# Kernel tuning notes

Measured on AMD Instinct MI355X. Metric: run time of the kernel, lower is better.

## Reference

```python
import jax, jax.numpy as jnp
import numpy as np

EPS = 1e-12
SIMILARITY = 'dot'  # non-tensor forward arg, closed over


def setup_inputs() -> dict:
    key = jax.random.key(0)
    k1, k2, k3, k4 = jax.random.split(key, 4)
    N, M, D = 4096, 8192, 512
    x = jax.random.normal(k1, (N, D), dtype=jnp.float32)
    x_n = jax.random.normal(k2, (M, D), dtype=jnp.float32)
    # Linear(D, 3) params
    W = jax.random.normal(k3, (3, D), dtype=jnp.float32) * (1.0 / np.sqrt(D))
    bias = jax.random.normal(k4, (3,), dtype=jnp.float32) * 0.01
    return {"x": x, "x_n": x_n, "W": W, "bias": bias}


def _sim_matrix(x, x_n, similarity):
    if similarity == 'l2':
        d2 = (jnp.sum(x * x, 1)[:, None] - 2.0 * (x @ x_n.T)
              + jnp.sum(x_n * x_n, 1)[None, :])
        return -jnp.sqrt(jnp.maximum(d2, 0.0))
    elif similarity == 'l1':
        return -jnp.sum(jnp.abs(x[:, None, :] - x_n[None, :, :]), axis=-1)
    elif similarity == 'dot':
        return (x @ x_n.T) / x.shape[1]
    elif similarity == 'cos':
        xn = x / jnp.linalg.norm(x, axis=1, keepdims=True)
        yn = x_n / jnp.linalg.norm(x_n, axis=1, keepdims=True)
        return xn @ yn.T


def reference(x, x_n, W, bias):
    # pointwise params from a Linear(D,3)+Sigmoid head, clamped to (eps, 1-eps)
    p = jnp.clip(jax.nn.sigmoid(x @ W.T + bias), EPS, 1.0 - EPS)  # [N,3]
    a = p[:, 0:1]
    b = p[:, 1:2]
    s = p[:, 2:3]
    b = a + b * (1.0 - a)

    sim = _sim_matrix(x, x_n, SIMILARITY)                # [N,M]
    smin = jnp.min(sim, axis=1, keepdims=True)
    smax = jnp.max(sim, axis=1, keepdims=True)
    sim_norm = (sim - smin) / (smax - smin)

    # x != x_n -> plain row max (torch.equal branch is False)
    top_sims = jnp.max(sim_norm, axis=1, keepdims=True)  # [N,1]
    a = jnp.minimum(a, top_sims) - EPS

    num = jnp.maximum(jnp.abs(sim_norm - a) ** (1.0 / s), EPS)
    denom = num + jnp.maximum(jnp.abs(b - sim_norm) ** (1.0 / s), EPS)
    soft_mask = num / denom

    lo = sim_norm < a
    hi = sim_norm > b
    soft_mask = jnp.where(lo, 0.0, jnp.where(hi, 1.0, soft_mask))
    # safe log: masked-to-0 entries give -inf forward, zero grad (matches torch)
    safe = jnp.where(lo, 1.0, soft_mask)
    log_mask = jnp.where(lo, -jnp.inf, jnp.log(safe))
    return sim + log_mask
```

## Files before the change

kernel.cpp:

```cpp
#include <hip/hip_runtime.h>
#include <hip/hip_fp16.h>
#include <math.h>

#define EPSF 1e-12f
#define NEG_HUGE (-1e30f)

typedef _Float16 half8_t __attribute__((ext_vector_type(8)));
typedef _Float16 half4_t __attribute__((ext_vector_type(4)));
typedef float floatx4 __attribute__((ext_vector_type(4)));

__device__ __forceinline__ float sigmoid_stable(float v) {
    if (v >= 0.0f) {
        return 1.0f / (1.0f + expf(-v));
    } else {
        float e = expf(v);
        return e / (1.0f + e);
    }
}

__global__ __launch_bounds__(64) void row_params_kernel(
    const float* __restrict__ x, const float* __restrict__ W,
    const float* __restrict__ bias,
    float* __restrict__ aeff, float* __restrict__ bnew, float* __restrict__ tinv)
{
    const int r = blockIdx.x;
    const int l = threadIdx.x;
    const float* xr = x + (size_t)r * 512;
    float s0 = 0.0f, s1 = 0.0f, s2 = 0.0f;
#pragma unroll
    for (int i = 0; i < 8; ++i) {
        int e = l * 8 + i;
        float xv = xr[e];
        s0 = fmaf(xv, W[e], s0);
        s1 = fmaf(xv, W[512 + e], s1);
        s2 = fmaf(xv, W[1024 + e], s2);
    }
#pragma unroll
    for (int off = 32; off > 0; off >>= 1) {
        s0 += __shfl_xor(s0, off);
        s1 += __shfl_xor(s1, off);
        s2 += __shfl_xor(s2, off);
    }
    if (l == 0) {
        float p0 = fminf(fmaxf(sigmoid_stable(s0 + bias[0]), EPSF), 1.0f);
        float p1 = fminf(fmaxf(sigmoid_stable(s1 + bias[1]), EPSF), 1.0f);
        float p2 = fminf(fmaxf(sigmoid_stable(s2 + bias[2]), EPSF), 1.0f);
        float b = p0 + p1 * (1.0f - p0);
        float ae = fminf(p0, 1.0f) - EPSF;
        aeff[r] = ae;
        bnew[r] = b;
        tinv[r] = 1.0f / p2;
    }
}

__global__ __launch_bounds__(256) void split_both_kernel(
    const float* __restrict__ x, const float* __restrict__ xn,
    _Float16* __restrict__ A2, _Float16* __restrict__ B2)
{
    int idx = blockIdx.x * 256 + threadIdx.x;
    int row = idx >> 7;
    int c = (idx & 127) << 2;
    const float* src;
    _Float16* dst;
    bool isB;
    if (row < 4096) {
        src = x + (size_t)row * 512 + c;
        dst = A2 + (size_t)row * 1536 + c;
        isB = false;
    } else {
        int r = row - 4096;
        src = xn + (size_t)r * 512 + c;
        dst = B2 + (size_t)r * 1536 + c;
        isB = true;
    }
    float4 v = *(const float4*)src;
    _Float16 h0 = (_Float16)v.x, h1 = (_Float16)v.y,
             h2 = (_Float16)v.z, h3 = (_Float16)v.w;
    half4_t hv = {h0, h1, h2, h3};
    half4_t lv = {(_Float16)(v.x - (float)h0), (_Float16)(v.y - (float)h1),
                  (_Float16)(v.z - (float)h2), (_Float16)(v.w - (float)h3)};
    *(half4_t*)(dst) = hv;
    *(half4_t*)(dst + 512)  = isB ? lv : hv;
    *(half4_t*)(dst + 1024) = isB ? hv : lv;
}

#define VMW_(N) asm volatile("s_waitcnt vmcnt(" #N ")" ::: "memory")
#define VMW(N) VMW_(N)
#define BARR() __builtin_amdgcn_s_barrier()

__device__ __forceinline__ void gload16(const _Float16* g, _Float16* l) {
    __builtin_amdgcn_global_load_lds(
        (const __attribute__((address_space(1))) unsigned int*)g,
        (__attribute__((address_space(3))) unsigned int*)l, 16, 0, 0);
}

#define RD_A4(dst, QQ, qd)                                                      \
    dst[0] = *(const half8_t*)(lds + (QQ)*16384 + ArdW + (2*(qd))*1024 + g0);   \
    dst[1] = *(const half8_t*)(lds + (QQ)*16384 + ArdW + (2*(qd))*1024 + g1);   \
    dst[2] = *(const half8_t*)(lds + (QQ)*16384 + ArdW + (2*(qd)+1)*1024 + g0); \
    dst[3] = *(const half8_t*)(lds + (QQ)*16384 + ArdW + (2*(qd)+1)*1024 + g1);

#define RD_B8(dst, QQ)                                                          \
    _Pragma("unroll")                                                           \
    for (int fn = 0; fn < 4; ++fn) {                                            \
        dst[2*fn]   = *(const half8_t*)(lds + (QQ)*16384 + BrdW + fn*1024 + g0);\
        dst[2*fn+1] = *(const half8_t*)(lds + (QQ)*16384 + BrdW + fn*1024 + g1);\
    }

#define MFMA_Q(qd, af, bf)                                                      \
    __builtin_amdgcn_s_setprio(1);                                              \
    _Pragma("unroll")                                                           \
    for (int fn = 0; fn < 4; ++fn) {                                            \
        acc[2*(qd)][fn] = __builtin_amdgcn_mfma_f32_16x16x32_f16(               \
            af[0], bf[2*fn], acc[2*(qd)][fn], 0, 0, 0);                         \
        acc[2*(qd)][fn] = __builtin_amdgcn_mfma_f32_16x16x32_f16(               \
            af[1], bf[2*fn+1], acc[2*(qd)][fn], 0, 0, 0);                       \
        acc[2*(qd)+1][fn] = __builtin_amdgcn_mfma_f32_16x16x32_f16(             \
            af[2], bf[2*fn], acc[2*(qd)+1][fn], 0, 0, 0);                       \
        acc[2*(qd)+1][fn] = __builtin_amdgcn_mfma_f32_16x16x32_f16(             \
            af[3], bf[2*fn+1], acc[2*(qd)+1][fn], 0, 0, 0);                     \
    }                                                                           \
    __builtin_amdgcn_s_setprio(0);

__global__ __launch_bounds__(512, 2) void mfma_gemm256_kernel(
    const _Float16* __restrict__ A, const _Float16* __restrict__ B,
    float* __restrict__ C,
    float* __restrict__ pmin, float* __restrict__ pmax)
{
    constexpr int KP = 1536;
    constexpr int NN = 8192;
    __shared__ __align__(16) _Float16 lds[65536];

    const int tid = threadIdx.x;
    const int wave = tid >> 6, lane = tid & 63;
    const int bx = blockIdx.x;
    const int by = blockIdx.y;
    const int wm = (wave >> 2) * 128;
    const int wn = (wave & 3) * 64;

    const int rl = lane & 15, lq = lane >> 4;
    const int rx7 = lane & 7;
    const int lrow = lane >> 3, gph = lane & 7;
    const int glog = gph ^ lrow;

    const _Float16* Bg = B + (size_t)(bx * 256 + wave * 8 + lrow) * KP + glog * 8;
    const _Float16* Ag = A + (size_t)(by * 256 + ((wave & 4) ? 128 : 0)
                                      + (wave & 3) * 8 + lrow) * KP + glog * 8;
    const int BdstW = 32768 + (wave * 8) * 64;
    const int AdstW = (((wave & 4) ? 128 : 0) + (wave & 3) * 8) * 64;
    const int ArdW = (wm + rl) * 64;
    const int BrdW = 32768 + (wn + rl) * 64;
    const int g0 = (lq ^ rx7) * 8;
    const int g1 = ((4 + lq) ^ rx7) * 8;

    floatx4 acc[8][4] = {};
    half8_t a0[4], a1[4], bA[8], bB[8];

    auto stageB = [&](int u, int qn, int kn) {
        gload16(Bg + (size_t)u * (64 * KP) + kn * 64,
                lds + qn * 16384 + BdstW + u * 4096);
    };
    auto stageA = [&](int s, int qn, int kn) {
        gload16(Ag + (size_t)s * (32 * KP) + kn * 64,
                lds + qn * 16384 + AdstW + s * 2048);
    };

#pragma unroll
    for (int u = 0; u < 4; ++u) stageB(u, 0, 0);
#pragma unroll
    for (int s = 0; s < 4; ++s) stageA(s, 0, 0);
    VMW(3);
    BARR();
    RD_B8(bA, 0); RD_A4(a0, 0, 0);
    stageB(0, 1, 1); stageB(1, 1, 1);
    VMW(4);
    BARR();

    for (int kt = 0; kt < 22; kt += 2) {
        const int k1 = kt + 1, k2 = kt + 2, k3 = kt + 3;
        RD_A4(a1, 0, 1); stageB(2, 1, k1); stageB(3, 1, k1);
        MFMA_Q(0, a0, bA); VMW(5); BARR();
        RD_A4(a0, 0, 2); stageA(0, 1, k1); stageA(1, 1, k1);
        MFMA_Q(1, a1, bA); VMW(6); BARR();
        RD_A4(a1, 0, 3); stageA(2, 1, k1); stageA(3, 1, k1);
        MFMA_Q(2, a0, bA); VMW(3); BARR();
        RD_B8(bB, 1); RD_A4(a0, 1, 0); stageB(0, 0, k2); stageB(1, 0, k2);
        MFMA_Q(3, a1, bA); VMW(4); BARR();
        RD_A4(a1, 1, 1); stageB(2, 0, k2); stageB(3, 0, k2);
        MFMA_Q(0, a0, bB); VMW(5); BARR();
        RD_A4(a0, 1, 2); stageA(0, 0, k2); stageA(1, 0, k2);
        MFMA_Q(1, a1, bB); VMW(6); BARR();
        RD_A4(a1, 1, 3); stageA(2, 0, k2); stageA(3, 0, k2);
        MFMA_Q(2, a0, bB); VMW(3); BARR();
        RD_B8(bA, 0); RD_A4(a0, 0, 0); stageB(0, 1, k3); stageB(1, 1, k3);
        MFMA_Q(3, a1, bB); VMW(4); BARR();
    }

    RD_A4(a1, 0, 1); stageB(2, 1, 23); stageB(3, 1, 23);
    MFMA_Q(0, a0, bA); VMW(5); BARR();
    RD_A4(a0, 0, 2); stageA(0, 1, 23); stageA(1, 1, 23);
    MFMA_Q(1, a1, bA); VMW(6); BARR();
    RD_A4(a1, 0, 3); stageA(2, 1, 23); stageA(3, 1, 23);
    MFMA_Q(2, a0, bA); VMW(3); BARR();
    RD_B8(bB, 1); RD_A4(a0, 1, 0);
    MFMA_Q(3, a1, bA); VMW(2); BARR();
    RD_A4(a1, 1, 1); MFMA_Q(0, a0, bB); VMW(1); BARR();
    RD_A4(a0, 1, 2); MFMA_Q(1, a1, bB); VMW(0); BARR();
    RD_A4(a1, 1, 3); MFMA_Q(2, a0, bB);
    MFMA_Q(3, a1, bB);

    const float sc = 1.0f / 512.0f;
    const int row0 = by * 256 + wm + lq * 4;
    const int col0 = bx * 256 + wn + rl;
    const int pslot = bx * 4 + (wave & 3);
#pragma unroll
    for (int fm = 0; fm < 8; ++fm) {
        float mn[4], mx[4];
#pragma unroll
        for (int r = 0; r < 4; ++r) {
            float* cp = C + (size_t)(row0 + fm * 16 + r) * NN + col0;
            float v0 = acc[fm][0][r] * sc, v1 = acc[fm][1][r] * sc;
            float v2 = acc[fm][2][r] * sc, v3 = acc[fm][3][r] * sc;
            cp[0] = v0; cp[16] = v1; cp[32] = v2; cp[48] = v3;
            mn[r] = fminf(fminf(v0, v1), fminf(v2, v3));
            mx[r] = fmaxf(fmaxf(v0, v1), fmaxf(v2, v3));
        }
#pragma unroll
        for (int off = 1; off < 16; off <<= 1)
#pragma unroll
            for (int r = 0; r < 4; ++r) {
                mn[r] = fminf(mn[r], __shfl_xor(mn[r], off));
                mx[r] = fmaxf(mx[r], __shfl_xor(mx[r], off));
            }
        if (rl == 0) {
#pragma unroll
            for (int r = 0; r < 4; ++r) {
                size_t row = (size_t)(row0 + fm * 16 + r);
                pmin[(row << 7) + pslot] = mn[r];
                pmax[(row << 7) + pslot] = mx[r];
            }
        }
    }
}

__global__ __launch_bounds__(64) void minmax_reduce_kernel(
    const float* __restrict__ pmin, const float* __restrict__ pmax,
    float* __restrict__ smin, float* __restrict__ smax)
{
    const int r = blockIdx.x;
    const int l = threadIdx.x;
    const float* bmin = pmin + ((size_t)r << 7);
    const float* bmax = pmax + ((size_t)r << 7);
    float mn = fminf(bmin[l], bmin[l + 64]);
    float mx = fmaxf(bmax[l], bmax[l + 64]);
#pragma unroll
    for (int off = 32; off > 0; off >>= 1) {
        mn = fminf(mn, __shfl_xor(mn, off));
        mx = fmaxf(mx, __shfl_xor(mx, off));
    }
    if (l == 0) {
        smin[r] = mn;
        smax[r] = mx;
    }
}

#define BM 128
#define BN 128
#define BK 16
__global__ __launch_bounds__(256) void sgemm_nt_kernel(
    const float* __restrict__ A, const float* __restrict__ B,
    float* __restrict__ C)
{
    const int K = 512;
    const int N = 8192;
    __shared__ float As[BK][BM];
    __shared__ float Bs[BK][BN];
    const int t = threadIdx.x;
    const int bx = blockIdx.x, by = blockIdx.y;
    const int m0 = t >> 2;
    const int kq = (t & 3) << 2;
    const float* Ap = A + ((size_t)(by * BM + m0) * K + kq);
    const float* Bp = B + ((size_t)(bx * BN + m0) * K + kq);
    const int tx = t & 15, ty = t >> 4;
    float acc[8][8] = {};
    float4 a0 = *(const float4*)(Ap), a1 = *(const float4*)(Ap + (size_t)64 * K);
    float4 b0 = *(const float4*)(Bp), b1 = *(const float4*)(Bp + (size_t)64 * K);
    for (int kt = 0; kt < K / BK; ++kt) {
        As[kq + 0][m0] = a0.x; As[kq + 1][m0] = a0.y; As[kq + 2][m0] = a0.z; As[kq + 3][m0] = a0.w;
        As[kq + 0][m0 + 64] = a1.x; As[kq + 1][m0 + 64] = a1.y; As[kq + 2][m0 + 64] = a1.z; As[kq + 3][m0 + 64] = a1.w;
        Bs[kq + 0][m0] = b0.x; Bs[kq + 1][m0] = b0.y; Bs[kq + 2][m0] = b0.z; Bs[kq + 3][m0] = b0.w;
        Bs[kq + 0][m0 + 64] = b1.x; Bs[kq + 1][m0 + 64] = b1.y; Bs[kq + 2][m0 + 64] = b1.z; Bs[kq + 3][m0 + 64] = b1.w;
        __syncthreads();
        if (kt + 1 < K / BK) {
            const float* Ap2 = Ap + (size_t)(kt + 1) * BK;
            const float* Bp2 = Bp + (size_t)(kt + 1) * BK;
            a0 = *(const float4*)(Ap2); a1 = *(const float4*)(Ap2 + (size_t)64 * K);
            b0 = *(const float4*)(Bp2); b1 = *(const float4*)(Bp2 + (size_t)64 * K);
        }
#pragma unroll
        for (int k = 0; k < BK; ++k) {
            float4 xa0 = *(const float4*)(&As[k][ty * 8]);
            float4 xa1 = *(const float4*)(&As[k][ty * 8 + 4]);
            float4 yb0 = *(const float4*)(&Bs[k][tx * 8]);
            float4 yb1 = *(const float4*)(&Bs[k][tx * 8 + 4]);
            float av[8] = {xa0.x, xa0.y, xa0.z, xa0.w, xa1.x, xa1.y, xa1.z, xa1.w};
            float bv[8] = {yb0.x, yb0.y, yb0.z, yb0.w, yb1.x, yb1.y, yb1.z, yb1.w};
#pragma unroll
            for (int i = 0; i < 8; ++i)
#pragma unroll
                for (int j = 0; j < 8; ++j)
                    acc[i][j] = fmaf(av[i], bv[j], acc[i][j]);
        }
        __syncthreads();
    }
    const float sc = 1.0f / 512.0f;
    const int gm = by * BM + ty * 8, gn = bx * BN + tx * 8;
#pragma unroll
    for (int i = 0; i < 8; ++i) {
        float4 o0 = make_float4(acc[i][0] * sc, acc[i][1] * sc, acc[i][2] * sc, acc[i][3] * sc);
        float4 o1 = make_float4(acc[i][4] * sc, acc[i][5] * sc, acc[i][6] * sc, acc[i][7] * sc);
        float* cp = C + (size_t)(gm + i) * N + gn;
        *(float4*)(cp) = o0;
        *(float4*)(cp + 4) = o1;
    }
}

__global__ __launch_bounds__(256) void row_minmax_kernel(
    const float* __restrict__ C, float* __restrict__ smin, float* __restrict__ smax)
{
    const int r = blockIdx.x;
    const float4* row = (const float4*)(C + (size_t)r * 8192);
    float mn = INFINITY, mx = -INFINITY;
#pragma unroll
    for (int i = 0; i < 8; ++i) {
        float4 v = row[threadIdx.x + i * 256];
        mn = fminf(mn, fminf(fminf(v.x, v.y), fminf(v.z, v.w)));
        mx = fmaxf(mx, fmaxf(fmaxf(v.x, v.y), fmaxf(v.z, v.w)));
    }
#pragma unroll
    for (int off = 32; off > 0; off >>= 1) {
        mn = fminf(mn, __shfl_xor(mn, off));
        mx = fmaxf(mx, __shfl_xor(mx, off));
    }
    __shared__ float smn[4], smx[4];
    if ((threadIdx.x & 63) == 0) {
        smn[threadIdx.x >> 6] = mn;
        smx[threadIdx.x >> 6] = mx;
    }
    __syncthreads();
    if (threadIdx.x == 0) {
        mn = fminf(fminf(smn[0], smn[1]), fminf(smn[2], smn[3]));
        mx = fmaxf(fmaxf(smx[0], smx[1]), fmaxf(smx[2], smx[3]));
        smin[r] = mn;
        smax[r] = mx;
    }
}

__device__ __forceinline__ float fast_pow(float x, float t) {
    return __expf(t * __logf(x));
}

__global__ __launch_bounds__(256) void epilogue_kernel(
    float* __restrict__ C,
    const float* __restrict__ aeff, const float* __restrict__ bnew,
    const float* __restrict__ tinv,
    const float* __restrict__ smin, const float* __restrict__ smax)
{
    const int r = blockIdx.y;
    const int c4 = blockIdx.x * 256 + threadIdx.x;
    const float a = aeff[r];
    const float b = bnew[r];
    const float t = tinv[r];
    const float mn = smin[r];
    const float range = smax[r] - mn;
    const float inv_range = (range > 0.0f) ? (1.0f / range) : 0.0f;

    floatx4* p = (floatx4*)(C + (size_t)r * 8192) + c4;
    floatx4 v = __builtin_nontemporal_load(p);
    floatx4 out;
#pragma unroll
    for (int i = 0; i < 4; ++i) {
        float sim = v[i];
        float sn = (sim - mn) * inv_range;
        float lm;
        if (sn < a) {
            lm = NEG_HUGE;
        } else if (sn > b) {
            lm = 0.0f;
        } else {
            float num = fmaxf(fast_pow(fabsf(sn - a), t), EPSF);
            float den = num + fmaxf(fast_pow(fabsf(b - sn), t), EPSF);
            lm = __logf(num / den);
        }
        out[i] = sim + lm;
    }
    __builtin_nontemporal_store(out, p);
}

extern "C" void kernel_launch(void* const* d_in, const int* in_sizes, int n_in,
                              void* d_out, int out_size, void* d_ws, size_t ws_size,
                              hipStream_t stream)
{
    const float* x    = (const float*)d_in[0];
    const float* x_n  = (const float*)d_in[1];
    const float* W    = (const float*)d_in[2];
    const float* bias = (const float*)d_in[3];
    float* C = (float*)d_out;
    float* ws = (float*)d_ws;

    float* aeff = ws;
    float* bnew = ws + 4096;
    float* tinv = ws + 8192;
    float* smin = ws + 12288;
    float* smax = ws + 16384;

    const size_t pmin_off = 128 * 1024;
    const size_t pbytes = (size_t)4096 * 128 * 4;
    const size_t a2_off = pmin_off + 2 * pbytes;
    const size_t a2_bytes = (size_t)4096 * 1536 * 2;
    const size_t b2_off = a2_off + a2_bytes;
    const size_t need = b2_off + (size_t)8192 * 1536 * 2;

    row_params_kernel<<<4096, 64, 0, stream>>>(x, W, bias, aeff, bnew, tinv);

    if (ws_size >= need) {
        float* pmin = (float*)((char*)d_ws + pmin_off);
        float* pmax = (float*)((char*)d_ws + pmin_off + pbytes);
        _Float16* A2 = (_Float16*)((char*)d_ws + a2_off);
        _Float16* B2 = (_Float16*)((char*)d_ws + b2_off);
        split_both_kernel<<<6144, 256, 0, stream>>>(x, x_n, A2, B2);
        mfma_gemm256_kernel<<<dim3(32, 16), 512, 0, stream>>>(A2, B2, C, pmin, pmax);
        minmax_reduce_kernel<<<4096, 64, 0, stream>>>(pmin, pmax, smin, smax);
    } else {
        sgemm_nt_kernel<<<dim3(8192 / BN, 4096 / BM), 256, 0, stream>>>(x, x_n, C);
        row_minmax_kernel<<<4096, 256, 0, stream>>>(C, smin, smax);
    }

    epilogue_kernel<<<dim3(8, 4096), 256, 0, stream>>>(C, aeff, bnew, tinv,
                                                       smin, smax);
}
```

Before: 295.6 us.

## Deepen GEMM prefetch to issue a full k-tile ahead

Restructures the double-buffered LDS pipeline in the similarity GEMM so the prologue stages both k-tiles 0 and 1, and each loop step loads the whole k+2 tile into the buffer that was just consumed. Vmcnt waits are raised so each barrier waits only on the older tile. The aim is to keep more global loads in flight and hide memory latency behind the MFMAs. The risk is that the larger outstanding-load counts and the reordered buffer reuse could cause LDS hazards if any wait count is wrong. It also moves more load issue into the first sub-steps of each tile.

```diff
diff --git a/kernel.cpp b/kernel.cpp
--- a/kernel.cpp
+++ b/kernel.cpp
@@ -169,39 +169,41 @@
     for (int u = 0; u < 4; ++u) stageB(u, 0, 0);
 #pragma unroll
     for (int s = 0; s < 4; ++s) stageA(s, 0, 0);
-    VMW(3);
+#pragma unroll
+    for (int u = 0; u < 4; ++u) stageB(u, 1, 1);
+#pragma unroll
+    for (int s = 0; s < 4; ++s) stageA(s, 1, 1);
+    VMW(11);
     BARR();
     RD_B8(bA, 0); RD_A4(a0, 0, 0);
-    stageB(0, 1, 1); stageB(1, 1, 1);
-    VMW(4);
+    VMW(10);
     BARR();
 
     for (int kt = 0; kt < 22; kt += 2) {
-        const int k1 = kt + 1, k2 = kt + 2, k3 = kt + 3;
-        RD_A4(a1, 0, 1); stageB(2, 1, k1); stageB(3, 1, k1);
-        MFMA_Q(0, a0, bA); VMW(5); BARR();
-        RD_A4(a0, 0, 2); stageA(0, 1, k1); stageA(1, 1, k1);
-        MFMA_Q(1, a1, bA); VMW(6); BARR();
-        RD_A4(a1, 0, 3); stageA(2, 1, k1); stageA(3, 1, k1);
-        MFMA_Q(2, a0, bA); VMW(3); BARR();
-        RD_B8(bB, 1); RD_A4(a0, 1, 0); stageB(0, 0, k2); stageB(1, 0, k2);
-        MFMA_Q(3, a1, bA); VMW(4); BARR();
-        RD_A4(a1, 1, 1); stageB(2, 0, k2); stageB(3, 0, k2);
-        MFMA_Q(0, a0, bB); VMW(5); BARR();
-        RD_A4(a0, 1, 2); stageA(0, 0, k2); stageA(1, 0, k2);
-        MFMA_Q(1, a1, bB); VMW(6); BARR();
-        RD_A4(a1, 1, 3); stageA(2, 0, k2); stageA(3, 0, k2);
-        MFMA_Q(2, a0, bB); VMW(3); BARR();
-        RD_B8(bA, 0); RD_A4(a0, 0, 0); stageB(0, 1, k3); stageB(1, 1, k3);
-        MFMA_Q(3, a1, bB); VMW(4); BARR();
-    }
-
-    RD_A4(a1, 0, 1); stageB(2, 1, 23); stageB(3, 1, 23);
-    MFMA_Q(0, a0, bA); VMW(5); BARR();
-    RD_A4(a0, 0, 2); stageA(0, 1, 23); stageA(1, 1, 23);
-    MFMA_Q(1, a1, bA); VMW(6); BARR();
-    RD_A4(a1, 0, 3); stageA(2, 1, 23); stageA(3, 1, 23);
-    MFMA_Q(2, a0, bA); VMW(3); BARR();
+        const int k2 = kt + 2, k3 = kt + 3;
+        RD_A4(a1, 0, 1);
+        stageB(0, 0, k2); stageB(1, 0, k2); stageB(2, 0, k2); stageB(3, 0, k2);
+        MFMA_Q(0, a0, bA); VMW(13); BARR();
+        RD_A4(a0, 0, 2); stageA(0, 0, k2); stageA(1, 0, k2);
+        MFMA_Q(1, a1, bA); VMW(14); BARR();
+        RD_A4(a1, 0, 3); stageA(2, 0, k2);
+        MFMA_Q(2, a0, bA); VMW(10); BARR();
+        RD_B8(bB, 1); RD_A4(a0, 1, 0); stageA(3, 0, k2);
+        MFMA_Q(3, a1, bA); VMW(10); BARR();
+        RD_A4(a1, 1, 1);
+        stageB(0, 1, k3); stageB(1, 1, k3); stageB(2, 1, k3); stageB(3, 1, k3);
+        MFMA_Q(0, a0, bB); VMW(13); BARR();
+        RD_A4(a0, 1, 2); stageA(0, 1, k3); stageA(1, 1, k3);
+        MFMA_Q(1, a1, bB); VMW(14); BARR();
+        RD_A4(a1, 1, 3); stageA(2, 1, k3);
+        MFMA_Q(2, a0, bB); VMW(10); BARR();
+        RD_B8(bA, 0); RD_A4(a0, 0, 0); stageA(3, 1, k3);
+        MFMA_Q(3, a1, bB); VMW(10); BARR();
+    }
+
+    RD_A4(a1, 0, 1); MFMA_Q(0, a0, bA); VMW(9); BARR();
+    RD_A4(a0, 0, 2); MFMA_Q(1, a1, bA); VMW(8); BARR();
+    RD_A4(a1, 0, 3); MFMA_Q(2, a0, bA); VMW(3); BARR();
     RD_B8(bB, 1); RD_A4(a0, 1, 0);
     MFMA_Q(3, a1, bA); VMW(2); BARR();
     RD_A4(a1, 1, 1); MFMA_Q(0, a0, bB); VMW(1); BARR();
```

New measurement: 295.6 us. Within noise of the previous version (-0.0%).

## Restructure GEMM main loop into ping-pong schedule with single fragment buffers

Applied to the files above, without the earlier changes.

Rewrites the k-loop of the fp16 MFMA GEMM to use one A and one B fragment register set, with explicit lgkmcnt waits and extra barriers around each MFMA quarter. This is meant to make waves alternate between LDS reads and MFMA bursts. The global-to-LDS staging is regrouped into half-tile loads of two 16-byte loads each, and the MFMA order inside each quarter is interleaved so consecutive MFMAs do not depend on each other. Dropping the double-buffered fragments lowers register pressure, but the extra barriers and LDS-read waits can leave MFMA idle where reads used to overlap compute.

```diff
diff --git a/kernel.cpp b/kernel.cpp
--- a/kernel.cpp
+++ b/kernel.cpp
@@ -87,6 +87,8 @@
 #define VMW_(N) asm volatile("s_waitcnt vmcnt(" #N ")" ::: "memory")
 #define VMW(N) VMW_(N)
 #define BARR() __builtin_amdgcn_s_barrier()
+#define LGKM0() asm volatile("s_waitcnt lgkmcnt(0)" ::: "memory")
+#define LGKM8() asm volatile("s_waitcnt lgkmcnt(8)" ::: "memory")
 
 __device__ __forceinline__ void gload16(const _Float16* g, _Float16* l) {
     __builtin_amdgcn_global_load_lds(
@@ -113,10 +115,13 @@
     for (int fn = 0; fn < 4; ++fn) {                                            \
         acc[2*(qd)][fn] = __builtin_amdgcn_mfma_f32_16x16x32_f16(               \
             af[0], bf[2*fn], acc[2*(qd)][fn], 0, 0, 0);                         \
+        acc[2*(qd)+1][fn] = __builtin_amdgcn_mfma_f32_16x16x32_f16(             \
+            af[2], bf[2*fn], acc[2*(qd)+1][fn], 0, 0, 0);                       \
+    }                                                                           \
+    _Pragma("unroll")                                                           \
+    for (int fn = 0; fn < 4; ++fn) {                                            \
         acc[2*(qd)][fn] = __builtin_amdgcn_mfma_f32_16x16x32_f16(               \
             af[1], bf[2*fn+1], acc[2*(qd)][fn], 0, 0, 0);                       \
-        acc[2*(qd)+1][fn] = __builtin_amdgcn_mfma_f32_16x16x32_f16(             \
-            af[2], bf[2*fn], acc[2*(qd)+1][fn], 0, 0, 0);                       \
         acc[2*(qd)+1][fn] = __builtin_amdgcn_mfma_f32_16x16x32_f16(             \
             af[3], bf[2*fn+1], acc[2*(qd)+1][fn], 0, 0, 0);                     \
     }                                                                           \
@@ -143,71 +148,79 @@
     const int lrow = lane >> 3, gph = lane & 7;
     const int glog = gph ^ lrow;
 
-    const _Float16* Bg = B + (size_t)(bx * 256 + wave * 8 + lrow) * KP + glog * 8;
-    const _Float16* Ag = A + (size_t)(by * 256 + ((wave & 4) ? 128 : 0)
-                                      + (wave & 3) * 8 + lrow) * KP + glog * 8;
-    const int BdstW = 32768 + (wave * 8) * 64;
-    const int AdstW = (((wave & 4) ? 128 : 0) + (wave & 3) * 8) * 64;
+    const _Float16* Ag2 = A + (size_t)(by * 256 + wave * 8 + lrow) * KP + glog * 8;
+    const _Float16* Bg2 = B + (size_t)(bx * 256 + wave * 8 + lrow) * KP + glog * 8;
     const int ArdW = (wm + rl) * 64;
     const int BrdW = 32768 + (wn + rl) * 64;
     const int g0 = (lq ^ rx7) * 8;
     const int g1 = ((4 + lq) ^ rx7) * 8;
 
     floatx4 acc[8][4] = {};
-    half8_t a0[4], a1[4], bA[8], bB[8];
-
-    auto stageB = [&](int u, int qn, int kn) {
-        gload16(Bg + (size_t)u * (64 * KP) + kn * 64,
-                lds + qn * 16384 + BdstW + u * 4096);
+    half8_t af[4], bfr[8];
+
+    auto stageA = [&](int half, int qn, int kn) {
+        const _Float16* s = Ag2 + (size_t)(half * 128) * KP + kn * 64;
+        _Float16* d = lds + qn * 16384 + (half * 128 + wave * 8) * 64;
+        gload16(s, d);
+        gload16(s + (size_t)64 * KP, d + 4096);
     };
-    auto stageA = [&](int s, int qn, int kn) {
-        gload16(Ag + (size_t)s * (32 * KP) + kn * 64,
-                lds + qn * 16384 + AdstW + s * 2048);
+    auto stageB = [&](int half, int qn, int kn) {
+        const _Float16* s = Bg2 + (size_t)(half * 128) * KP + kn * 64;
+        _Float16* d = lds + 32768 + qn * 16384 + (half * 128 + wave * 8) * 64;
+        gload16(s, d);
+        gload16(s + (size_t)64 * KP, d + 4096);
     };
 
-#pragma unroll
-    for (int u = 0; u < 4; ++u) stageB(u, 0, 0);
-#pragma unroll
-    for (int s = 0; s < 4; ++s) stageA(s, 0, 0);
-    VMW(3);
-    BARR();
-    RD_B8(bA, 0); RD_A4(a0, 0, 0);
+    stageB(0, 0, 0); stageB(1, 0, 0);
+    stageA(0, 0, 0); stageA(1, 0, 0);
     stageB(0, 1, 1); stageB(1, 1, 1);
     VMW(4);
     BARR();
 
     for (int kt = 0; kt < 22; kt += 2) {
         const int k1 = kt + 1, k2 = kt + 2, k3 = kt + 3;
-        RD_A4(a1, 0, 1); stageB(2, 1, k1); stageB(3, 1, k1);
-        MFMA_Q(0, a0, bA); VMW(5); BARR();
-        RD_A4(a0, 0, 2); stageA(0, 1, k1); stageA(1, 1, k1);
-        MFMA_Q(1, a1, bA); VMW(6); BARR();
-        RD_A4(a1, 0, 3); stageA(2, 1, k1); stageA(3, 1, k1);
-        MFMA_Q(2, a0, bA); VMW(3); BARR();
-        RD_B8(bB, 1); RD_A4(a0, 1, 0); stageB(0, 0, k2); stageB(1, 0, k2);
-        MFMA_Q(3, a1, bA); VMW(4); BARR();
-        RD_A4(a1, 1, 1); stageB(2, 0, k2); stageB(3, 0, k2);
-        MFMA_Q(0, a0, bB); VMW(5); BARR();
-        RD_A4(a0, 1, 2); stageA(0, 0, k2); stageA(1, 0, k2);
-        MFMA_Q(1, a1, bB); VMW(6); BARR();
-        RD_A4(a1, 1, 3); stageA(2, 0, k2); stageA(3, 0, k2);
-        MFMA_Q(2, a0, bB); VMW(3); BARR();
-        RD_B8(bA, 0); RD_A4(a0, 0, 0); stageB(0, 1, k3); stageB(1, 1, k3);
-        MFMA_Q(3, a1, bB); VMW(4); BARR();
-    }
-
-    RD_A4(a1, 0, 1); stageB(2, 1, 23); stageB(3, 1, 23);
-    MFMA_Q(0, a0, bA); VMW(5); BARR();
-    RD_A4(a0, 0, 2); stageA(0, 1, 23); stageA(1, 1, 23);
-    MFMA_Q(1, a1, bA); VMW(6); BARR();
-    RD_A4(a1, 0, 3); stageA(2, 1, 23); stageA(3, 1, 23);
-    MFMA_Q(2, a0, bA); VMW(3); BARR();
-    RD_B8(bB, 1); RD_A4(a0, 1, 0);
-    MFMA_Q(3, a1, bA); VMW(2); BARR();
-    RD_A4(a1, 1, 1); MFMA_Q(0, a0, bB); VMW(1); BARR();
-    RD_A4(a0, 1, 2); MFMA_Q(1, a1, bB); VMW(0); BARR();
-    RD_A4(a1, 1, 3); MFMA_Q(2, a0, bB);
-    MFMA_Q(3, a1, bB);
+        RD_B8(bfr, 0); RD_A4(af, 0, 0); stageA(0, 1, k1);
+        LGKM8(); BARR(); LGKM0();
+        MFMA_Q(0, af, bfr); BARR();
+        RD_A4(af, 0, 1); stageA(1, 1, k1);
+        BARR(); LGKM0();
+        MFMA_Q(1, af, bfr); BARR();
+        RD_A4(af, 0, 2); stageB(0, 0, k2);
+        BARR(); LGKM0();
+        MFMA_Q(2, af, bfr); BARR();
+        RD_A4(af, 0, 3); stageB(1, 0, k2);
+        BARR(); LGKM0();
+        MFMA_Q(3, af, bfr); VMW(4); BARR();
+        RD_B8(bfr, 1); RD_A4(af, 1, 0); stageA(0, 0, k2);
+        LGKM8(); BARR(); LGKM0();
+        MFMA_Q(0, af, bfr); BARR();
+        RD_A4(af, 1, 1); stageA(1, 0, k2);
+        BARR(); LGKM0();
+        MFMA_Q(1, af, bfr); BARR();
+        RD_A4(af, 1, 2); stageB(0, 1, k3);
+        BARR(); LGKM0();
+        MFMA_Q(2, af, bfr); BARR();
+        RD_A4(af, 1, 3); stageB(1, 1, k3);
+        BARR(); LGKM0();
+        MFMA_Q(3, af, bfr); VMW(4); BARR();
+    }
+
+    RD_B8(bfr, 0); RD_A4(af, 0, 0); stageA(0, 1, 23);
+    LGKM8(); BARR(); LGKM0(); MFMA_Q(0, af, bfr); BARR();
+    RD_A4(af, 0, 1); stageA(1, 1, 23);
+    BARR(); LGKM0(); MFMA_Q(1, af, bfr); BARR();
+    RD_A4(af, 0, 2);
+    BARR(); LGKM0(); MFMA_Q(2, af, bfr); BARR();
+    RD_A4(af, 0, 3);
+    BARR(); LGKM0(); MFMA_Q(3, af, bfr); VMW(0); BARR();
+    RD_B8(bfr, 1); RD_A4(af, 1, 0);
+    BARR(); LGKM0(); MFMA_Q(0, af, bfr); BARR();
+    RD_A4(af, 1, 1);
+    BARR(); LGKM0(); MFMA_Q(1, af, bfr); BARR();
+    RD_A4(af, 1, 2);
+    BARR(); LGKM0(); MFMA_Q(2, af, bfr); BARR();
+    RD_A4(af, 1, 3);
+    LGKM0(); MFMA_Q(3, af, bfr);
 
     const float sc = 1.0f / 512.0f;
     const int row0 = by * 256 + wm + lq * 4;
```

Measured after the change: 296.4 us. About the same (+0.3%).

## Fuse gate params into split kernel and min/max reduce into epilogue; reorder MFMAs

Applied to the files above, without the earlier changes.

Folds the Linear+sigmoid row-parameter computation into the fp16 split kernel, so x is read once and one launch goes away. Merges the per-row partial min/max reduction into a per-row epilogue kernel, removing another launch and the separate smin/smax round trip. Also reorders the MFMA issue so consecutive instructions hit independent accumulators, which should reduce dependency stalls. The trade-offs are an extra __syncthreads in the split kernel and a different grid shape for the epilogue, one block per row looping over 8 vectors per thread.

```diff
diff --git a/kernel.cpp b/kernel.cpp
--- a/kernel.cpp
+++ b/kernel.cpp
@@ -53,10 +53,13 @@
     }
 }
 
-__global__ __launch_bounds__(256) void split_both_kernel(
+__global__ __launch_bounds__(256) void split_gates_kernel(
     const float* __restrict__ x, const float* __restrict__ xn,
-    _Float16* __restrict__ A2, _Float16* __restrict__ B2)
-{
+    const float* __restrict__ W, const float* __restrict__ bias,
+    _Float16* __restrict__ A2, _Float16* __restrict__ B2,
+    float* __restrict__ aeff, float* __restrict__ bnew, float* __restrict__ tinv)
+{
+    __shared__ float sred[3][4];
     int idx = blockIdx.x * 256 + threadIdx.x;
     int row = idx >> 7;
     int c = (idx & 127) << 2;
@@ -82,6 +85,38 @@
     *(half4_t*)(dst) = hv;
     *(half4_t*)(dst + 512)  = isB ? lv : hv;
     *(half4_t*)(dst + 1024) = isB ? hv : lv;
+
+    if (!isB) {
+        float s0 = v.x * W[c] + v.y * W[c + 1] + v.z * W[c + 2] + v.w * W[c + 3];
+        float s1 = v.x * W[512 + c] + v.y * W[513 + c]
+                 + v.z * W[514 + c] + v.w * W[515 + c];
+        float s2 = v.x * W[1024 + c] + v.y * W[1025 + c]
+                 + v.z * W[1026 + c] + v.w * W[1027 + c];
+#pragma unroll
+        for (int off = 32; off > 0; off >>= 1) {
+            s0 += __shfl_xor(s0, off);
+            s1 += __shfl_xor(s1, off);
+            s2 += __shfl_xor(s2, off);
+        }
+        const int w = threadIdx.x >> 6;
+        if ((threadIdx.x & 63) == 0) {
+            sred[0][w] = s0; sred[1][w] = s1; sred[2][w] = s2;
+        }
+        __syncthreads();
+        if ((threadIdx.x & 127) == 0) {
+            const int w0 = threadIdx.x >> 6;
+            float t0 = sred[0][w0] + sred[0][w0 + 1];
+            float t1 = sred[1][w0] + sred[1][w0 + 1];
+            float t2 = sred[2][w0] + sred[2][w0 + 1];
+            float p0 = fminf(fmaxf(sigmoid_stable(t0 + bias[0]), EPSF), 1.0f);
+            float p1 = fminf(fmaxf(sigmoid_stable(t1 + bias[1]), EPSF), 1.0f);
+            float p2 = fminf(fmaxf(sigmoid_stable(t2 + bias[2]), EPSF), 1.0f);
+            float b = p0 + p1 * (1.0f - p0);
+            aeff[row] = fminf(p0, 1.0f) - EPSF;
+            bnew[row] = b;
+            tinv[row] = 1.0f / p2;
+        }
+    }
 }
 
 #define VMW_(N) asm volatile("s_waitcnt vmcnt(" #N ")" ::: "memory")
@@ -113,10 +148,13 @@
     for (int fn = 0; fn < 4; ++fn) {                                            \
         acc[2*(qd)][fn] = __builtin_amdgcn_mfma_f32_16x16x32_f16(               \
             af[0], bf[2*fn], acc[2*(qd)][fn], 0, 0, 0);                         \
+        acc[2*(qd)+1][fn] = __builtin_amdgcn_mfma_f32_16x16x32_f16(             \
+            af[2], bf[2*fn], acc[2*(qd)+1][fn], 0, 0, 0);                       \
+    }                                                                           \
+    _Pragma("unroll")                                                           \
+    for (int fn = 0; fn < 4; ++fn) {                                            \
         acc[2*(qd)][fn] = __builtin_amdgcn_mfma_f32_16x16x32_f16(               \
             af[1], bf[2*fn+1], acc[2*(qd)][fn], 0, 0, 0);                       \
-        acc[2*(qd)+1][fn] = __builtin_amdgcn_mfma_f32_16x16x32_f16(             \
-            af[2], bf[2*fn], acc[2*(qd)+1][fn], 0, 0, 0);                       \
         acc[2*(qd)+1][fn] = __builtin_amdgcn_mfma_f32_16x16x32_f16(             \
             af[3], bf[2*fn+1], acc[2*(qd)+1][fn], 0, 0, 0);                     \
     }                                                                           \
@@ -243,24 +281,63 @@
     }
 }
 
-__global__ __launch_bounds__(64) void minmax_reduce_kernel(
-    const float* __restrict__ pmin, const float* __restrict__ pmax,
-    float* __restrict__ smin, float* __restrict__ smax)
+__device__ __forceinline__ float fast_pow(float x, float t) {
+    return __expf(t * __logf(x));
+}
+
+__global__ __launch_bounds__(256) void epilogue_row_kernel(
+    float* __restrict__ C,
+    const float* __restrict__ aeff, const float* __restrict__ bnew,
+    const float* __restrict__ tinv,
+    const float* __restrict__ pmin, const float* __restrict__ pmax)
 {
     const int r = blockIdx.x;
-    const int l = threadIdx.x;
-    const float* bmin = pmin + ((size_t)r << 7);
-    const float* bmax = pmax + ((size_t)r << 7);
-    float mn = fminf(bmin[l], bmin[l + 64]);
-    float mx = fmaxf(bmax[l], bmax[l + 64]);
+    const int t = threadIdx.x;
+    __shared__ float smn[4], smx[4];
+    float mn = INFINITY, mx = -INFINITY;
+    if (t < 128) {
+        mn = pmin[((size_t)r << 7) + t];
+        mx = pmax[((size_t)r << 7) + t];
+    }
 #pragma unroll
     for (int off = 32; off > 0; off >>= 1) {
         mn = fminf(mn, __shfl_xor(mn, off));
         mx = fmaxf(mx, __shfl_xor(mx, off));
     }
-    if (l == 0) {
-        smin[r] = mn;
-        smax[r] = mx;
+    if ((t & 63) == 0) { smn[t >> 6] = mn; smx[t >> 6] = mx; }
+    __syncthreads();
+    const float rmn = fminf(smn[0], smn[1]);
+    const float rmx = fmaxf(smx[0], smx[1]);
+
+    const float a = aeff[r];
+    const float b = bnew[r];
+    const float tv = tinv[r];
+    const float range = rmx - rmn;
+    const float inv_range = (range > 0.0f) ? (1.0f / range) : 0.0f;
+
+    floatx4* prow = (floatx4*)(C + (size_t)r * 8192);
+#pragma unroll
+    for (int i = 0; i < 8; ++i) {
+        floatx4* p = prow + t + i * 256;
+        floatx4 v = __builtin_nontemporal_load(p);
+        floatx4 out;
+#pragma unroll
+        for (int j = 0; j < 4; ++j) {
+            float sim = v[j];
+            float sn = (sim - rmn) * inv_range;
+            float lm;
+            if (sn < a) {
+                lm = NEG_HUGE;
+            } else if (sn > b) {
+                lm = 0.0f;
+            } else {
+                float num = fmaxf(fast_pow(fabsf(sn - a), tv), EPSF);
+                float den = num + fmaxf(fast_pow(fabsf(b - sn), tv), EPSF);
+                lm = __logf(num / den);
+            }
+            out[j] = sim + lm;
+        }
+        __builtin_nontemporal_store(out, p);
     }
 }
 
@@ -356,10 +433,6 @@
     }
 }
 
-__device__ __forceinline__ float fast_pow(float x, float t) {
-    return __expf(t * __logf(x));
-}
-
 __global__ __launch_bounds__(256) void epilogue_kernel(
     float* __restrict__ C,
     const float* __restrict__ aeff, const float* __restrict__ bnew,
@@ -421,21 +494,21 @@
     const size_t b2_off = a2_off + a2_bytes;
     const size_t need = b2_off + (size_t)8192 * 1536 * 2;
 
-    row_params_kernel<<<4096, 64, 0, stream>>>(x, W, bias, aeff, bnew, tinv);
-
     if (ws_size >= need) {
         float* pmin = (float*)((char*)d_ws + pmin_off);
         float* pmax = (float*)((char*)d_ws + pmin_off + pbytes);
         _Float16* A2 = (_Float16*)((char*)d_ws + a2_off);
         _Float16* B2 = (_Float16*)((char*)d_ws + b2_off);
-        split_both_kernel<<<6144, 256, 0, stream>>>(x, x_n, A2, B2);
+        split_gates_kernel<<<6144, 256, 0, stream>>>(x, x_n, W, bias, A2, B2,
+                                                     aeff, bnew, tinv);
         mfma_gemm256_kernel<<<dim3(32, 16), 512, 0, stream>>>(A2, B2, C, pmin, pmax);
-        minmax_reduce_kernel<<<4096, 64, 0, stream>>>(pmin, pmax, smin, smax);
+        epilogue_row_kernel<<<4096, 256, 0, stream>>>(C, aeff, bnew, tinv,
+                                                      pmin, pmax);
     } else {
+        row_params_kernel<<<4096, 64, 0, stream>>>(x, W, bias, aeff, bnew, tinv);
         sgemm_nt_kernel<<<dim3(8192 / BN, 4096 / BM), 256, 0, stream>>>(x, x_n, C);
         row_minmax_kernel<<<4096, 256, 0, stream>>>(C, smin, smax);
-    }
-
-    epilogue_kernel<<<dim3(8, 4096), 256, 0, stream>>>(C, aeff, bnew, tinv,
-                                                       smin, smax);
-}
+        epilogue_kernel<<<dim3(8, 4096), 256, 0, stream>>>(C, aeff, bnew, tinv,
+                                                           smin, smax);
+    }
+}
```

New measurement: 293.9 us. Within noise of the previous version (-0.6%).
